# Kernel optimization log

Measured on AMD Instinct MI355X. Metric: run time of the kernel, lower is better.

## Reference

```python
import jax, jax.numpy as jnp
import numpy as np
from jax import lax

FEAT = 256      # feat_channels
GROUPS = 32     # GN num_groups
NCLS = 80       # num_classes - 1
NRAYS = 36      # polar mask rays
STACK = 4       # stacked_convs
SIZES = [(160, 256), (80, 128), (40, 64), (20, 32), (10, 16)]
B = 1


def conv(x, w, b=None):
    # 3x3 conv, stride 1, pad 1 (SAME). x: [N,C,H,W], w: [O,I,3,3]
    y = lax.conv_general_dilated(x, w, (1, 1), 'SAME',
                                 dimension_numbers=('NCHW', 'OIHW', 'NCHW'))
    if b is not None:
        y = y + b[None, :, None, None]
    return y


def group_norm(x, g, b, eps=1e-5):
    N, C, H, W = x.shape
    xr = x.reshape(N, GROUPS, C // GROUPS, H, W)
    m = xr.mean(axis=(2, 3, 4), keepdims=True)
    v = xr.var(axis=(2, 3, 4), keepdims=True)
    xr = (xr - m) * jax.lax.rsqrt(v + eps)
    return xr.reshape(N, C, H, W) * g[None, :, None, None] + b[None, :, None, None]


def tower(x, ws, gs, bs):
    # ConvModule: conv (no bias, norm present) -> GN -> ReLU, repeated STACK times
    for i in range(STACK):
        x = jax.nn.relu(group_norm(conv(x, ws[i]), gs[i], bs[i]))
    return x


def setup_inputs() -> dict:
    key = jax.random.key(0)
    ks = jax.random.split(key, 32)
    d = {}
    for l, (h, w) in enumerate(SIZES):
        d[f'feat{l}'] = jax.random.normal(ks[l], (B, FEAT, h, w), dtype=jnp.float32)
    std = 0.01
    for j, name in enumerate(['cls', 'reg', 'msk']):
        d[f'{name}_w'] = jax.random.normal(ks[5 + j], (STACK, FEAT, FEAT, 3, 3), jnp.float32) * std
        d[f'{name}_g'] = jnp.ones((STACK, FEAT), jnp.float32)
        d[f'{name}_b'] = jnp.zeros((STACK, FEAT), jnp.float32)
    bias_cls = float(-np.log((1 - 0.01) / 0.01))  # bias_init_with_prob(0.01)
    d['pcls_w'] = jax.random.normal(ks[10], (NCLS, FEAT, 3, 3), jnp.float32) * std
    d['pcls_b'] = jnp.full((NCLS,), bias_cls, jnp.float32)
    d['preg_w'] = jax.random.normal(ks[11], (4, FEAT, 3, 3), jnp.float32) * std
    d['preg_b'] = jnp.zeros((4,), jnp.float32)
    d['pmsk_w'] = jax.random.normal(ks[12], (NRAYS, FEAT, 3, 3), jnp.float32) * std
    d['pmsk_b'] = jnp.zeros((NRAYS,), jnp.float32)
    d['pctr_w'] = jax.random.normal(ks[13], (1, FEAT, 3, 3), jnp.float32) * std
    d['pctr_b'] = jnp.zeros((1,), jnp.float32)
    d['scales_bbox'] = jnp.ones((5,), jnp.float32)
    d['scales_mask'] = jnp.ones((5,), jnp.float32)
    return d


def reference(feat0, feat1, feat2, feat3, feat4,
              cls_w, cls_g, cls_b, reg_w, reg_g, reg_b, msk_w, msk_g, msk_b,
              pcls_w, pcls_b, preg_w, preg_b, pmsk_w, pmsk_b, pctr_w, pctr_b,
              scales_bbox, scales_mask):
    feats = [feat0, feat1, feat2, feat3, feat4]
    cls_outs, bbox_outs, ctr_outs, mask_outs = [], [], [], []
    for l, x in enumerate(feats):
        cf = tower(x, cls_w, cls_g, cls_b)
        cls_outs.append(conv(cf, pcls_w, pcls_b))
        ctr_outs.append(conv(cf, pctr_w, pctr_b))
        rf = tower(x, reg_w, reg_g, reg_b)
        bbox_outs.append(jnp.exp(conv(rf, preg_w, preg_b) * scales_bbox[l]))
        mf = tower(x, msk_w, msk_g, msk_b)
        mask_outs.append(jnp.exp(conv(mf, pmsk_w, pmsk_b) * scales_mask[l]))
    # multi_apply grouping: (cls_scores, bbox_preds, centernesses, mask_preds)
    return tuple(cls_outs) + tuple(bbox_outs) + tuple(ctr_outs) + tuple(mask_outs)
```

## Files before the change

### kernel.cpp

```cpp
#include <hip/hip_runtime.h>

typedef unsigned short u16;
typedef unsigned int u32;
typedef short bf16x8 __attribute__((ext_vector_type(8)));
typedef float f32x4 __attribute__((ext_vector_type(4)));

__device__ __forceinline__ float bf2f(u16 u) {
  u32 x = ((u32)u) << 16;
  float f;
  __builtin_memcpy(&f, &x, 4);
  return f;
}
__device__ __forceinline__ u16 f2bf(float f) {
  u32 x;
  __builtin_memcpy(&x, &f, 4);
  u32 r = x + 0x7FFFu + ((x >> 16) & 1u);
  return (u16)(r >> 16);
}
__device__ __forceinline__ void glds16(const u16* g, u16* l) {
  __builtin_amdgcn_global_load_lds((const __attribute__((address_space(1))) u32*)g,
                                   (__attribute__((address_space(3))) u32*)l, 16, 0, 0);
}


__global__ void convert_weights(const float* __restrict__ cw, const float* __restrict__ rw,
                                const float* __restrict__ mw, const float* __restrict__ pc,
                                const float* __restrict__ pr, const float* __restrict__ pm,
                                const float* __restrict__ pt, u16* __restrict__ dst) {
  int e = blockIdx.x * 256 + threadIdx.x;
  if (e >= 7446528) return;
  float v = 0.f;
  if (e < 7077888) {
    int conv = e / 589824, r = e % 589824;
    int mo = r / 294912;
    int r2 = r - mo * 294912;
    int kt = r2 >> 12;
    int r3 = r2 & 4095;
    int wm = r3 >> 11;
    int mi = (r3 >> 9) & 3;
    int l = (r3 >> 3) & 63;
    int j = r3 & 7;
    int ch = kt / 9, tap = kt - ch * 9;
    int o = mo * 128 + wm * 64 + mi * 16 + (l & 15);
    int c = ch * 32 + (l >> 4) * 8 + j;
    const float* s = (conv < 4) ? cw : (conv < 8) ? rw : mw;
    int si = conv & 3;
    v = s[((si * 256 + o) * 256 + c) * 9 + tap];
  } else {
    int e2 = e - 7077888;
    if (e2 < 221184) {
      int chunk = e2 / 27648, r = e2 % 27648;
      int tap = r / 3072, r2 = r % 3072;
      int g = r2 / 768;
      int o = (r2 - g * 768) >> 3;
      int c = chunk * 32 + g * 8 + (r2 & 7);
      if (o < 80) v = pc[(o * 256 + c) * 9 + tap];
      else if (o == 80) v = pt[c * 9 + tap];
    } else if (e2 < 258048) {
      int e3 = e2 - 221184;
      int chunk = e3 / 4608, r = e3 % 4608;
      int tap = r / 512, r2 = r % 512;
      int g = r2 >> 7;
      int o = (r2 >> 3) & 15;
      int c = chunk * 32 + g * 8 + (r2 & 7);
      if (o < 4) v = pr[(o * 256 + c) * 9 + tap];
    } else {
      int e3 = e2 - 258048;
      int chunk = e3 / 13824, r = e3 % 13824;
      int tap = r / 1536, r2 = r % 1536;
      int g = r2 / 384;
      int o = (r2 - g * 384) >> 3;
      int c = chunk * 32 + g * 8 + (r2 & 7);
      if (o < 36) v = pm[(o * 256 + c) * 9 + tap];
    }
  }
  dst[e] = f2bf(v);
}

__global__ void halo_zero(u16* __restrict__ X, u16* __restrict__ Y, long ACT, int ntw) {
  int i = blockIdx.x * 256 + threadIdx.x;
  int rep = i / 26112;
  int j = i - rep * 26112;
  if (rep >= 2 * ntw) return;
  int hp = j >> 4, sub = j & 15;
  int Wp, Hp, pxb, h;
  if (hp < 836)       { Wp = 258; Hp = 162; pxb = 0;     h = hp; }
  else if (hp < 1256) { Wp = 130; Hp = 82;  pxb = 41796; h = hp - 836; }
  else if (hp < 1468) { Wp = 66;  Hp = 42;  pxb = 52456; h = hp - 1256; }
  else if (hp < 1576) { Wp = 34;  Hp = 22;  pxb = 55228; h = hp - 1468; }
  else                { Wp = 18;  Hp = 12;  pxb = 55976; h = hp - 1576; }
  int y, x;
  if (h < Wp)          { y = 0;      x = h; }
  else if (h < 2 * Wp) { y = Hp - 1; x = h - Wp; }
  else {
    int rr = h - 2 * Wp;
    y = 1 + (rr >> 1);
    x = (rr & 1) ? (Wp - 1) : 0;
  }
  u16* buf = (rep < ntw) ? (X + rep * ACT) : (Y + (rep - ntw) * ACT);
  long adr = (long)(pxb + y * Wp + x) * 256 + sub * 16;
  uint4 z = {0, 0, 0, 0};
  *(uint4*)(buf + adr) = z;
  *(uint4*)(buf + adr + 8) = z;
}

__global__ void feat_to_nhwc(const float* __restrict__ f0, const float* __restrict__ f1,
                             const float* __restrict__ f2, const float* __restrict__ f3,
                             const float* __restrict__ f4, u16* __restrict__ dst,
                             long tstride, int nrep) {
  __shared__ float lds[64 * 65];
  int bx = blockIdx.x;
  int tile = bx >> 2, c0 = (bx & 3) * 64;
  int tl, sh, pxb, npx;
  const float* src;
  if (tile < 640)      { tl = tile;       sh = 8; pxb = 0;     npx = 40960; src = f0; }
  else if (tile < 800) { tl = tile - 640; sh = 7; pxb = 41796; npx = 10240; src = f1; }
  else if (tile < 840) { tl = tile - 800; sh = 6; pxb = 52456; npx = 2560;  src = f2; }
  else if (tile < 850) { tl = tile - 840; sh = 5; pxb = 55228; npx = 640;   src = f3; }
  else                 { tl = tile - 850; sh = 4; pxb = 55976; npx = 160;   src = f4; }
  int W = 1 << sh, Wp = W + 2;
  int px0 = tl * 64;
  int t = threadIdx.x;
  {
    int cc = (t >> 6) * 16, px = t & 63;
    bool ok = (px0 + px) < npx;
#pragma unroll
    for (int j = 0; j < 16; ++j) {
      float v = ok ? src[(c0 + cc + j) * npx + px0 + px] : 0.f;
      lds[(cc + j) * 65 + px] = v;
    }
  }
  __syncthreads();
  {
    int px = t >> 2, cL = (t & 3) * 16;
    int pxi = px0 + px;
    if (pxi < npx) {
      int y = pxi >> sh, x = pxi & (W - 1);
      u32 w[8];
#pragma unroll
      for (int j = 0; j < 8; ++j) {
        u16 a = f2bf(lds[(cL + 2 * j) * 65 + px]);
        u16 b = f2bf(lds[(cL + 2 * j + 1) * 65 + px]);
        w[j] = (u32)a | ((u32)b << 16);
      }
      long adr = (long)(pxb + (y + 1) * Wp + (x + 1)) * 256 + c0 + cL;
      uint4 v0 = {w[0], w[1], w[2], w[3]}, v1 = {w[4], w[5], w[6], w[7]};
      for (int r = 0; r < nrep; ++r) {
        *(uint4*)(dst + r * tstride + adr) = v0;
        *(uint4*)(dst + r * tstride + adr + 8) = v1;
      }
    }
  }
}

__global__ void finalize_stats(const float* __restrict__ stats, int st_ts,
                               const float* __restrict__ g0, const float* __restrict__ g1,
                               const float* __restrict__ g2, const float* __restrict__ b0,
                               const float* __restrict__ b1, const float* __restrict__ b2,
                               float* __restrict__ scaleb, int sb_ts, int ntw) {
  int i = blockIdx.x * 256 + threadIdx.x;
  if (i >= ntw * 1280) return;
  int tw = i / 1280, r = i - tw * 1280, lvl = r >> 8, c = r & 255, g = c >> 3;
  float cnt = (lvl == 0) ? 327680.f : (lvl == 1) ? 81920.f
              : (lvl == 2) ? 20480.f : (lvl == 3) ? 5120.f : 1280.f;
  float s1 = stats[tw * st_ts + (lvl * 32 + g) * 2];
  float s2 = stats[tw * st_ts + (lvl * 32 + g) * 2 + 1];
  float mean = s1 / cnt;
  float var = s2 / cnt - mean * mean;
  float inv = rsqrtf(fmaxf(var, 0.f) + 1e-5f);
  const float* ga = (tw == 0) ? g0 : (tw == 1) ? g1 : g2;
  const float* be = (tw == 0) ? b0 : (tw == 1) ? b1 : b2;
  float sc = inv * ga[c];
  scaleb[(long)tw * sb_ts + (lvl * 256 + c) * 2] = sc;
  scaleb[(long)tw * sb_ts + (lvl * 256 + c) * 2 + 1] = be[c] - mean * sc;
}

__global__ __launch_bounds__(256, 3) void conv_tower(
    const u16* __restrict__ Xn, long in_ts, const u16* __restrict__ Wt, long wt_ts,
    u16* __restrict__ Yraw, long out_ts, float* __restrict__ stats, int st_ts,
    const float* __restrict__ scaleb, int sb_ts, int do_gn) {
  __shared__ __align__(16) u16 Btile[7200];
  __shared__ float shSB[512];
  __shared__ float sred[32];
  int bx = blockIdx.x;
  int tw = bx / 856, r856 = bx - tw * 856;
  Xn += tw * in_ts; Wt += tw * wt_ts; Yraw += tw * out_ts; stats += tw * st_ts;
  int tile = r856 >> 1, mo = r856 & 1;
  int tloc, W, H, SX, pxb, lvl;
  if (tile < 320)      { lvl = 0; tloc = tile;       W = 256; H = 160; SX = 4; pxb = 0; }
  else if (tile < 400) { lvl = 1; tloc = tile - 320; W = 128; H = 80;  SX = 3; pxb = 41796; }
  else if (tile < 420) { lvl = 2; tloc = tile - 400; W = 64;  H = 40;  SX = 2; pxb = 52456; }
  else if (tile < 426) { lvl = 3; tloc = tile - 420; W = 32;  H = 20;  SX = 1; pxb = 55228; }
  else                 { lvl = 4; tloc = tile - 426; W = 16;  H = 10;  SX = 0; pxb = 55976; }
  int Wp = W + 2;
  int ty = tloc >> SX, txi = tloc & ((1 << SX) - 1);
  int y0 = ty * 8, x0 = txi * 16;
  int t = threadIdx.x, lane = t & 63, wave = t >> 6;
  int wm = wave >> 1, wn = wave & 1;
  int quad = lane >> 4, col = lane & 15;
  const u16* Xbase = Xn + (long)(pxb + y0 * Wp + x0) * 256;
  const u16* Wb = Wt + (long)mo * 294912 + wm * 2048 + (long)lane * 8;
  int bcol = wn * 2880 + col * 40 + quad * 8;
  if (do_gn) {
    float2 sv = *(const float2*)(scaleb + (long)tw * sb_ts + (lvl * 256 + t) * 2);
    *(float2*)(&shSB[t * 2]) = sv;
  }
  bf16x8 areg[2][4];
#pragma unroll
  for (int mi = 0; mi < 4; ++mi) areg[0][mi] = *(const bf16x8*)(Wb + mi * 512);
  f32x4 acc[4][4] = {};
  for (int ch = 0; ch < 8; ++ch) {
    __syncthreads();
#pragma unroll
    for (int i = 0; i < 3; ++i) {
      int u = t + i * 256;
      if (u < 720) {
        int p = u >> 2, q = u & 3;
        int py = p / 18, px = p - py * 18;
        uint4 v = *(const uint4*)(Xbase + (long)(py * Wp + px) * 256 + ch * 32 + q * 8);
        if (do_gn) {
          int cb = ch * 32 + q * 8;
          int yg = y0 + py, xg = x0 + px;
          bool keep = (yg >= 1) && (yg <= H) && (xg >= 1) && (xg <= W);
          float4 s01 = *(const float4*)(&shSB[cb * 2]);
          float4 s23 = *(const float4*)(&shSB[cb * 2 + 4]);
          float4 s45 = *(const float4*)(&shSB[cb * 2 + 8]);
          float4 s67 = *(const float4*)(&shSB[cb * 2 + 12]);
          u32 wv[4] = {v.x, v.y, v.z, v.w};
          float sc[8] = {s01.x, s01.z, s23.x, s23.z, s45.x, s45.z, s67.x, s67.z};
          float bi[8] = {s01.y, s01.w, s23.y, s23.w, s45.y, s45.w, s67.y, s67.w};
          u32 ow[4];
#pragma unroll
          for (int jj = 0; jj < 4; ++jj) {
            float f0 = bf2f((u16)(wv[jj] & 0xffff)) * sc[2 * jj] + bi[2 * jj];
            float f1 = bf2f((u16)(wv[jj] >> 16)) * sc[2 * jj + 1] + bi[2 * jj + 1];
            f0 = keep ? fmaxf(f0, 0.f) : 0.f;
            f1 = keep ? fmaxf(f1, 0.f) : 0.f;
            ow[jj] = (u32)f2bf(f0) | ((u32)f2bf(f1) << 16);
          }
          v.x = ow[0]; v.y = ow[1]; v.z = ow[2]; v.w = ow[3];
        }
        *(uint4*)(Btile + p * 40 + q * 8) = v;
      }
    }
    __syncthreads();
#pragma unroll
    for (int tap = 0; tap < 9; ++tap) {
      int kt = ch * 9 + tap;
      if (kt < 71) {
        const u16* wn_ = Wb + (long)(kt + 1) * 4096;
#pragma unroll
        for (int mi = 0; mi < 4; ++mi)
          areg[(tap + 1) & 1][mi] = *(const bf16x8*)(wn_ + mi * 512);
      }
      int dy = tap / 3, dx = tap - dy * 3;
      int bb = bcol + dy * 720 + dx * 40;
#pragma unroll
      for (int ni = 0; ni < 4; ++ni) {
        bf16x8 b = *(const bf16x8*)(Btile + bb + ni * 720);
#pragma unroll
        for (int mi = 0; mi < 4; ++mi)
          acc[mi][ni] =
              __builtin_amdgcn_mfma_f32_16x16x32_bf16(areg[tap & 1][mi], b, acc[mi][ni], 0, 0, 0);
      }
    }
#pragma unroll
    for (int mi = 0; mi < 4; ++mi) areg[0][mi] = areg[1][mi];
  }
  if (t < 32) sred[t] = 0.f;
  __syncthreads();
  long pebase = (long)(pxb + (y0 + 1) * Wp + (x0 + col + 1)) * 256;
#pragma unroll
  for (int ni = 0; ni < 4; ++ni) {
    int row = wn * 4 + ni;
    if (y0 + row < H) {
#pragma unroll
      for (int mi = 0; mi < 4; ++mi) {
        f32x4 v = acc[mi][ni];
        int o = mo * 128 + wm * 64 + mi * 16 + quad * 4;
        ushort4 pk;
        pk.x = f2bf(v[0]); pk.y = f2bf(v[1]); pk.z = f2bf(v[2]); pk.w = f2bf(v[3]);
        *(ushort4*)(Yraw + pebase + (long)row * Wp * 256 + o) = pk;
      }
    }
  }
#pragma unroll
  for (int mi = 0; mi < 4; ++mi) {
    float s1 = 0.f, s2 = 0.f;
#pragma unroll
    for (int ni = 0; ni < 4; ++ni) {
      if (y0 + wn * 4 + ni < H) {
        f32x4 v = acc[mi][ni];
#pragma unroll
        for (int r2 = 0; r2 < 4; ++r2) { float f = v[r2]; s1 += f; s2 += f * f; }
      }
    }
#pragma unroll
    for (int m = 1; m < 16; m <<= 1) { s1 += __shfl_xor(s1, m); s2 += __shfl_xor(s2, m); }
    if (col == 0) {
      int g = (wm * 64 + mi * 16 + quad * 4) >> 3;
      atomicAdd(&sred[g * 2], s1);
      atomicAdd(&sred[g * 2 + 1], s2);
    }
  }
  __syncthreads();
  if (t < 32) atomicAdd(&stats[(lvl * 32 + mo * 16 + (t >> 1)) * 2 + (t & 1)], sred[t]);
}

__global__ void gn_relu(u16* __restrict__ buf, long tstride,
                        const float* __restrict__ scaleb, int sb_ts) {
  int i = blockIdx.x * 256 + threadIdx.x;
  int tw = i / 1745920;
  int j = i - tw * 1745920;
  buf += tw * tstride;
  const float* sbp = scaleb + (long)tw * sb_ts;
  int px = j >> 5, cg = j & 31, c0 = cg << 3;
  int lvl, sh, pxb, rem;
  if (px < 40960)      { lvl = 0; rem = px;         sh = 8; pxb = 0;     }
  else if (px < 51200) { lvl = 1; rem = px - 40960; sh = 7; pxb = 41796; }
  else if (px < 53760) { lvl = 2; rem = px - 51200; sh = 6; pxb = 52456; }
  else if (px < 54400) { lvl = 3; rem = px - 53760; sh = 5; pxb = 55228; }
  else                 { lvl = 4; rem = px - 54400; sh = 4; pxb = 55976; }
  int W = 1 << sh;
  int y = rem >> sh, x = rem & (W - 1);
  long adr = (long)(pxb + (y + 1) * (W + 2) + (x + 1)) * 256 + c0;
  uint4 rv = *(const uint4*)(buf + adr);
  const float* pc = sbp + (lvl * 256 + c0) * 2;
  float4 q0 = *(const float4*)(pc);
  float4 q1 = *(const float4*)(pc + 4);
  float4 q2 = *(const float4*)(pc + 8);
  float4 q3 = *(const float4*)(pc + 12);
  float sc[8] = {q0.x, q0.z, q1.x, q1.z, q2.x, q2.z, q3.x, q3.z};
  float bi[8] = {q0.y, q0.w, q1.y, q1.w, q2.y, q2.w, q3.y, q3.w};
  u32 w[4] = {rv.x, rv.y, rv.z, rv.w};
  u32 ow[4];
#pragma unroll
  for (int jj = 0; jj < 4; ++jj) {
    float v0 = fmaxf(bf2f((u16)(w[jj] & 0xffff)) * sc[2 * jj] + bi[2 * jj], 0.f);
    float v1 = fmaxf(bf2f((u16)(w[jj] >> 16)) * sc[2 * jj + 1] + bi[2 * jj + 1], 0.f);
    ow[jj] = (u32)f2bf(v0) | ((u32)f2bf(v1) << 16);
  }
  uint4 sv = {ow[0], ow[1], ow[2], ow[3]};
  *(uint4*)(buf + adr) = sv;
}

__global__ __launch_bounds__(256, 2) void conv_head_fused(
    const u16* __restrict__ Xbase, long ACT, int htsel, const u16* __restrict__ Whead,
    float* __restrict__ out, const float* __restrict__ pcb, const float* __restrict__ ptb,
    const float* __restrict__ prb, const float* __restrict__ pmb,
    const float* __restrict__ sb, const float* __restrict__ sm) {
  __shared__ u16 Alds[3072];
  __shared__ u16 Blds[2048];
  int bx = blockIdx.x;
  int ht, r;
  if (htsel >= 0) { ht = htsel; r = bx; }
  else { ht = bx / 853; r = bx - ht * 853; }
  int mt, woff;
  const float* bias0;
  const float* scl;
  if (ht == 0)      { mt = 96; woff = 0;      bias0 = pcb; scl = sb; }
  else if (ht == 1) { mt = 16; woff = 221184; bias0 = prb; scl = sb; }
  else              { mt = 48; woff = 258048; bias0 = pmb; scl = sm; }
  const u16* Xn = Xbase + ((htsel >= 0) ? 0 : (long)ht * ACT);
  const u16* Wh = Whead + woff;
  int mt32 = mt * 32, MI = mt >> 4;
  int lvl, tloc, W, H, SX, pxb, npx;
  if (r < 640)      { lvl = 0; tloc = r;       W = 256; H = 160; SX = 4; pxb = 0;     npx = 40960; }
  else if (r < 800) { lvl = 1; tloc = r - 640; W = 128; H = 80;  SX = 3; pxb = 41796; npx = 10240; }
  else if (r < 840) { lvl = 2; tloc = r - 800; W = 64;  H = 40;  SX = 2; pxb = 52456; npx = 2560;  }
  else if (r < 850) { lvl = 3; tloc = r - 840; W = 32;  H = 20;  SX = 1; pxb = 55228; npx = 640;   }
  else              { lvl = 4; tloc = r - 850; W = 16;  H = 10;  SX = 0; pxb = 55976; npx = 160;   }
  int obm, obc = 0;
  if (ht == 0) {
    const int obms[5] = {0, 3276800, 4096000, 4300800, 4352000};
    const int obcs[5] = {4583040, 4624000, 4634240, 4636800, 4637440};
    obm = obms[lvl]; obc = obcs[lvl];
  } else if (ht == 1) {
    const int obms[5] = {4364800, 4528640, 4569600, 4579840, 4582400};
    obm = obms[lvl];
  } else {
    const int obms[5] = {4637600, 6112160, 6480800, 6572960, 6596000};
    obm = obms[lvl];
  }
  int Wp = W + 2;
  int ty = tloc >> SX, txi = tloc & ((1 << SX) - 1);
  int y0 = ty * 4, x0 = txi * 16;
  int t = threadIdx.x, lane = t & 63, wave = t >> 6;
  int quad = lane >> 4, col = lane & 15;
  bool edge = (y0 + 5 > H + 1);
  int rr = (t & 63) >> 4, cc = t & 15, gg = t >> 6;
  const u16* Xrow = Xn + (long)(pxb + (y0 + rr) * Wp + (x0 + cc)) * 256 + gg * 8;
  int aoff = quad * (mt * 8) + col * 8;
  int boff = quad * 512 + (wave * 16 + col) * 8;
  f32x4 acc[6] = {};
  for (int ch = 0; ch < 8; ++ch) {
#pragma unroll
    for (int tap = 0; tap < 9; ++tap) {
      int dy = tap / 3, dx = tap - dy * 3;
      const u16* ws = Wh + (ch * 9 + tap) * mt32;
      int ta = t * 8;
      if (ta < mt32) glds16(ws + ta, Alds + ta);
      int tb = ta + 2048;
      if (tb < mt32) glds16(ws + tb, Alds + tb);
      const u16* xsrc = Xrow + ch * 32 + (dy * Wp + dx) * 256;
      if (!edge) {
        glds16(xsrc, Blds + t * 8);
      } else {
        int yp = y0 + rr + dy;
        uint4 v = {0, 0, 0, 0};
        if (yp <= H + 1) v = *(const uint4*)xsrc;
        *(uint4*)(Blds + t * 8) = v;
      }
      __syncthreads();
      bf16x8 b = *(const bf16x8*)(Blds + boff);
#pragma unroll
      for (int mi = 0; mi < 6; ++mi) {
        if (mi < MI) {
          bf16x8 a = *(const bf16x8*)(Alds + aoff + mi * 128);
          acc[mi] = __builtin_amdgcn_mfma_f32_16x16x32_bf16(a, b, acc[mi], 0, 0, 0);
        }
      }
      __syncthreads();
    }
  }
  int y = y0 + wave;
  if (y < H) {
    float sc = scl[lvl];
    int x = x0 + col;
#pragma unroll
    for (int mi = 0; mi < 6; ++mi) {
      if (mi < MI) {
#pragma unroll
        for (int r2 = 0; r2 < 4; ++r2) {
          int o = mi * 16 + quad * 4 + r2;
          float v = acc[mi][r2];
          if (ht == 0) {
            if (o < 80) out[obm + o * npx + y * W + x] = v + bias0[o];
            else if (o == 80) out[obc + y * W + x] = v + ptb[0];
          } else if (ht == 1) {
            if (o < 4) out[obm + o * npx + y * W + x] = expf((v + bias0[o]) * sc);
          } else {
            if (o < 36) out[obm + o * npx + y * W + x] = expf((v + bias0[o]) * sc);
          }
        }
      }
    }
  }
}

extern "C" void kernel_launch(void* const* d_in, const int* in_sizes, int n_in,
                              void* d_out, int out_size, void* d_ws, size_t ws_size,
                              hipStream_t stream) {
  const float* feat0 = (const float*)d_in[0];
  const float* feat1 = (const float*)d_in[1];
  const float* feat2 = (const float*)d_in[2];
  const float* feat3 = (const float*)d_in[3];
  const float* feat4 = (const float*)d_in[4];
  const float* cw = (const float*)d_in[5];
  const float* rw = (const float*)d_in[8];
  const float* mw = (const float*)d_in[11];
  const float* gmas[3] = {(const float*)d_in[6], (const float*)d_in[9], (const float*)d_in[12]};
  const float* btas[3] = {(const float*)d_in[7], (const float*)d_in[10], (const float*)d_in[13]};
  const float* pcw = (const float*)d_in[14];
  const float* pcb = (const float*)d_in[15];
  const float* prw = (const float*)d_in[16];
  const float* prb = (const float*)d_in[17];
  const float* pmw = (const float*)d_in[18];
  const float* pmb = (const float*)d_in[19];
  const float* ptw = (const float*)d_in[20];
  const float* ptb = (const float*)d_in[21];
  const float* sb = (const float*)d_in[22];
  const float* sm = (const float*)d_in[23];
  float* out = (float*)d_out;

  const long ACT = 14385152;
  const long ACTB = 28770304;
  const long WTS = 14893056;
  char* base = (char*)d_ws;
  u16* wts = (u16*)base;

  size_t need_fused = WTS + 6 * (size_t)ACTB + 3840 + 30720 + 65536;

  convert_weights<<<29088, 256, 0, stream>>>(cw, rw, mw, pcw, prw, pmw, ptw, wts);

  if (ws_size >= need_fused) {
    u16* X = (u16*)(base + WTS);
    u16* Y = (u16*)(base + WTS + 3 * ACTB);
    float* stats = (float*)(base + WTS + 6 * ACTB);
    float* scaleb = (float*)(base + WTS + 6 * ACTB + 3840);
    halo_zero<<<612, 256, 0, stream>>>(X, Y, ACT, 3);
    feat_to_nhwc<<<3412, 256, 0, stream>>>(feat0, feat1, feat2, feat3, feat4, X, ACT, 1);
    for (int s = 0; s < 4; ++s) {
      u16* in = (s & 1) ? Y : X;
      u16* ot = (s & 1) ? X : Y;
      long ints = (s == 0) ? 0 : ACT;
      hipMemsetAsync(stats, 0, 3840, stream);
      conv_tower<<<2568, 256, 0, stream>>>(in, ints, wts + s * 589824, 4 * 589824, ot, ACT,
                                           stats, 320, scaleb, 2560, s > 0);
      finalize_stats<<<15, 256, 0, stream>>>(stats, 320,
                                             gmas[0] + s * 256, gmas[1] + s * 256, gmas[2] + s * 256,
                                             btas[0] + s * 256, btas[1] + s * 256, btas[2] + s * 256,
                                             scaleb, 2560, 3);
    }
    gn_relu<<<20460, 256, 0, stream>>>(X, ACT, scaleb, 2560);
    conv_head_fused<<<2559, 256, 0, stream>>>(X, ACT, -1, wts + 7077888, out,
                                              pcb, ptb, prb, pmb, sb, sm);
  } else {
    u16* bufA = (u16*)(base + WTS);
    u16* bufB = (u16*)(base + WTS + ACTB);
    float* stats = (float*)(base + WTS + 2 * ACTB);
    float* scaleb = (float*)(base + WTS + 2 * ACTB + 1280);
    halo_zero<<<204, 256, 0, stream>>>(bufA, bufB, 0, 1);
    for (int tw = 0; tw < 3; ++tw) {
      feat_to_nhwc<<<3412, 256, 0, stream>>>(feat0, feat1, feat2, feat3, feat4, bufA, 0, 1);
      for (int s = 0; s < 4; ++s) {
        u16* in = (s & 1) ? bufB : bufA;
        u16* ot = (s & 1) ? bufA : bufB;
        hipMemsetAsync(stats, 0, 1280, stream);
        conv_tower<<<856, 256, 0, stream>>>(in, 0, wts + (tw * 4 + s) * 589824, 0, ot, 0,
                                            stats, 0, scaleb, 0, s > 0);
        finalize_stats<<<5, 256, 0, stream>>>(stats, 0,
                                              gmas[tw] + s * 256, gmas[tw] + s * 256, gmas[tw] + s * 256,
                                              btas[tw] + s * 256, btas[tw] + s * 256, btas[tw] + s * 256,
                                              scaleb, 0, 1);
      }
      gn_relu<<<6820, 256, 0, stream>>>(bufA, 0, scaleb, 0);
      conv_head_fused<<<853, 256, 0, stream>>>(bufA, 0, tw, wts + 7077888, out,
                                               pcb, ptb, prb, pmb, sb, sm);
    }
  }
}
```

Baseline: 1.146 ms.

## Prefetch next input chunk into registers, relayout B tile, cheaper bf16 packing

The conv tower kernel now issues the global loads for the next 32-channel chunk into registers right after the LDS barrier, so their latency overlaps the MFMA work of the current chunk. Per-thread address, LDS offset and border-mask math is hoisted out of the channel loop. The LDS B tile is reorganised into quad-major planes with no padding, which shrinks it from 7200 to 5760 elements. The f32-to-bf16 round-to-nearest-even conversion is replaced by a round-half-up add plus byte permute, which costs fewer instructions but breaks ties differently and may change bank-conflict behaviour.

```diff
diff --git a/kernel.cpp b/kernel.cpp
--- a/kernel.cpp
+++ b/kernel.cpp
@@ -16,6 +16,14 @@
   __builtin_memcpy(&x, &f, 4);
   u32 r = x + 0x7FFFu + ((x >> 16) & 1u);
   return (u16)(r >> 16);
+}
+__device__ __forceinline__ u32 pack2(float f0, float f1) {
+  u32 a, b;
+  __builtin_memcpy(&a, &f0, 4);
+  __builtin_memcpy(&b, &f1, 4);
+  a += 0x8000u;
+  b += 0x8000u;
+  return __builtin_amdgcn_perm(b, a, 0x07060302);
 }
 __device__ __forceinline__ void glds16(const u16* g, u16* l) {
   __builtin_amdgcn_global_load_lds((const __attribute__((address_space(1))) u32*)g,
@@ -138,11 +146,8 @@
       int y = pxi >> sh, x = pxi & (W - 1);
       u32 w[8];
 #pragma unroll
-      for (int j = 0; j < 8; ++j) {
-        u16 a = f2bf(lds[(cL + 2 * j) * 65 + px]);
-        u16 b = f2bf(lds[(cL + 2 * j + 1) * 65 + px]);
-        w[j] = (u32)a | ((u32)b << 16);
-      }
+      for (int j = 0; j < 8; ++j)
+        w[j] = pack2(lds[(cL + 2 * j) * 65 + px], lds[(cL + 2 * j + 1) * 65 + px]);
       long adr = (long)(pxb + (y + 1) * Wp + (x + 1)) * 256 + c0 + cL;
       uint4 v0 = {w[0], w[1], w[2], w[3]}, v1 = {w[4], w[5], w[6], w[7]};
       for (int r = 0; r < nrep; ++r) {
@@ -179,7 +184,7 @@
     const u16* __restrict__ Xn, long in_ts, const u16* __restrict__ Wt, long wt_ts,
     u16* __restrict__ Yraw, long out_ts, float* __restrict__ stats, int st_ts,
     const float* __restrict__ scaleb, int sb_ts, int do_gn) {
-  __shared__ __align__(16) u16 Btile[7200];
+  __shared__ __align__(16) u16 Btile[5760];
   __shared__ float shSB[512];
   __shared__ float sred[32];
   int bx = blockIdx.x;
@@ -200,11 +205,30 @@
   int quad = lane >> 4, col = lane & 15;
   const u16* Xbase = Xn + (long)(pxb + y0 * Wp + x0) * 256;
   const u16* Wb = Wt + (long)mo * 294912 + wm * 2048 + (long)lane * 8;
-  int bcol = wn * 2880 + col * 40 + quad * 8;
+  int bcol = quad * 1440 + wn * 576 + col * 8;
   if (do_gn) {
     float2 sv = *(const float2*)(scaleb + (long)tw * sb_ts + (lvl * 256 + t) * 2);
     *(float2*)(&shSB[t * 2]) = sv;
   }
+  const u16* Pptr[3];
+  int Lo[3], Cb[3];
+  bool Uok[3], Keep[3];
+#pragma unroll
+  for (int i = 0; i < 3; ++i) {
+    int u = t + i * 256;
+    Uok[i] = u < 720;
+    int q = u & 3, p = u >> 2;
+    int py = p / 18, px = p - py * 18;
+    Pptr[i] = Xbase + (long)(py * Wp + px) * 256 + q * 8;
+    Lo[i] = q * 1440 + p * 8;
+    Cb[i] = q * 8;
+    int yg = y0 + py, xg = x0 + px;
+    Keep[i] = (yg >= 1) && (yg <= H) && (xg >= 1) && (xg <= W);
+  }
+  uint4 breg[3];
+#pragma unroll
+  for (int i = 0; i < 3; ++i)
+    if (Uok[i]) breg[i] = *(const uint4*)(Pptr[i]);
   bf16x8 areg[2][4];
 #pragma unroll
   for (int mi = 0; mi < 4; ++mi) areg[0][mi] = *(const bf16x8*)(Wb + mi * 512);
@@ -213,37 +237,38 @@
     __syncthreads();
 #pragma unroll
     for (int i = 0; i < 3; ++i) {
-      int u = t + i * 256;
-      if (u < 720) {
-        int p = u >> 2, q = u & 3;
-        int py = p / 18, px = p - py * 18;
-        uint4 v = *(const uint4*)(Xbase + (long)(py * Wp + px) * 256 + ch * 32 + q * 8);
+      if (Uok[i]) {
+        uint4 v = breg[i];
         if (do_gn) {
-          int cb = ch * 32 + q * 8;
-          int yg = y0 + py, xg = x0 + px;
-          bool keep = (yg >= 1) && (yg <= H) && (xg >= 1) && (xg <= W);
-          float4 s01 = *(const float4*)(&shSB[cb * 2]);
-          float4 s23 = *(const float4*)(&shSB[cb * 2 + 4]);
-          float4 s45 = *(const float4*)(&shSB[cb * 2 + 8]);
-          float4 s67 = *(const float4*)(&shSB[cb * 2 + 12]);
+          int cb2 = (Cb[i] + ch * 32) * 2;
+          float4 s01 = *(const float4*)(&shSB[cb2]);
+          float4 s23 = *(const float4*)(&shSB[cb2 + 4]);
+          float4 s45 = *(const float4*)(&shSB[cb2 + 8]);
+          float4 s67 = *(const float4*)(&shSB[cb2 + 12]);
           u32 wv[4] = {v.x, v.y, v.z, v.w};
           float sc[8] = {s01.x, s01.z, s23.x, s23.z, s45.x, s45.z, s67.x, s67.z};
           float bi[8] = {s01.y, s01.w, s23.y, s23.w, s45.y, s45.w, s67.y, s67.w};
+          bool kp = Keep[i];
           u32 ow[4];
 #pragma unroll
           for (int jj = 0; jj < 4; ++jj) {
             float f0 = bf2f((u16)(wv[jj] & 0xffff)) * sc[2 * jj] + bi[2 * jj];
             float f1 = bf2f((u16)(wv[jj] >> 16)) * sc[2 * jj + 1] + bi[2 * jj + 1];
-            f0 = keep ? fmaxf(f0, 0.f) : 0.f;
-            f1 = keep ? fmaxf(f1, 0.f) : 0.f;
-            ow[jj] = (u32)f2bf(f0) | ((u32)f2bf(f1) << 16);
+            f0 = kp ? fmaxf(f0, 0.f) : 0.f;
+            f1 = kp ? fmaxf(f1, 0.f) : 0.f;
+            ow[jj] = pack2(f0, f1);
           }
           v.x = ow[0]; v.y = ow[1]; v.z = ow[2]; v.w = ow[3];
         }
-        *(uint4*)(Btile + p * 40 + q * 8) = v;
+        *(uint4*)(Btile + Lo[i]) = v;
       }
     }
     __syncthreads();
+    if (ch < 7) {
+#pragma unroll
+      for (int i = 0; i < 3; ++i)
+        if (Uok[i]) breg[i] = *(const uint4*)(Pptr[i] + (ch + 1) * 32);
+    }
 #pragma unroll
     for (int tap = 0; tap < 9; ++tap) {
       int kt = ch * 9 + tap;
@@ -254,10 +279,10 @@
           areg[(tap + 1) & 1][mi] = *(const bf16x8*)(wn_ + mi * 512);
       }
       int dy = tap / 3, dx = tap - dy * 3;
-      int bb = bcol + dy * 720 + dx * 40;
+      int bb = bcol + dy * 144 + dx * 8;
 #pragma unroll
       for (int ni = 0; ni < 4; ++ni) {
-        bf16x8 b = *(const bf16x8*)(Btile + bb + ni * 720);
+        bf16x8 b = *(const bf16x8*)(Btile + bb + ni * 144);
 #pragma unroll
         for (int mi = 0; mi < 4; ++mi)
           acc[mi][ni] =
@@ -278,9 +303,10 @@
       for (int mi = 0; mi < 4; ++mi) {
         f32x4 v = acc[mi][ni];
         int o = mo * 128 + wm * 64 + mi * 16 + quad * 4;
-        ushort4 pk;
-        pk.x = f2bf(v[0]); pk.y = f2bf(v[1]); pk.z = f2bf(v[2]); pk.w = f2bf(v[3]);
-        *(ushort4*)(Yraw + pebase + (long)row * Wp * 256 + o) = pk;
+        uint2 pk;
+        pk.x = pack2(v[0], v[1]);
+        pk.y = pack2(v[2], v[3]);
+        *(uint2*)(Yraw + pebase + (long)row * Wp * 256 + o) = pk;
       }
     }
   }
@@ -338,7 +364,7 @@
   for (int jj = 0; jj < 4; ++jj) {
     float v0 = fmaxf(bf2f((u16)(w[jj] & 0xffff)) * sc[2 * jj] + bi[2 * jj], 0.f);
     float v1 = fmaxf(bf2f((u16)(w[jj] >> 16)) * sc[2 * jj + 1] + bi[2 * jj + 1], 0.f);
-    ow[jj] = (u32)f2bf(v0) | ((u32)f2bf(v1) << 16);
+    ow[jj] = pack2(v0, v1);
   }
   uint4 sv = {ow[0], ow[1], ow[2], ow[3]};
   *(uint4*)(buf + adr) = sv;
```

New measurement: 1.129 ms. No clear change (-1.4%).
